# Performance work log

Measured on AMD Instinct MI355X. Metric: run time of the kernel, lower is better.

Reference implementation:

```python
import jax, jax.numpy as jnp
import numpy as np

D_MODEL = 1024
N_HEADS = 16
HEAD_DIM = D_MODEL // N_HEADS
D_FF = 4 * D_MODEL
LN_EPS = 1e-5  # torch nn.LayerNorm default


def setup_inputs() -> dict:
    key = jax.random.key(0)
    ks = jax.random.split(key, 6)
    B, T = 2, 2048
    s = lambda fan_in: 1.0 / np.sqrt(fan_in)
    return {
        "x": jax.random.normal(ks[0], (B, T, D_MODEL), dtype=jnp.float32),
        # weights stored as [in, out]
        "w_qkv": jax.random.normal(ks[1], (D_MODEL, 3 * D_MODEL), dtype=jnp.float32) * s(D_MODEL),
        "w_proj": jax.random.normal(ks[2], (D_MODEL, D_MODEL), dtype=jnp.float32) * s(D_MODEL),
        "ln1_g": jnp.ones((D_MODEL,), jnp.float32),
        "ln1_b": jnp.zeros((D_MODEL,), jnp.float32),
        "ln2_g": jnp.ones((D_MODEL,), jnp.float32),
        "ln2_b": jnp.zeros((D_MODEL,), jnp.float32),
        "w_ff1": jax.random.normal(ks[3], (D_MODEL, D_FF), dtype=jnp.float32) * s(D_MODEL),
        "b_ff1": jnp.zeros((D_FF,), jnp.float32),
        "w_ff2": jax.random.normal(ks[4], (D_FF, D_MODEL), dtype=jnp.float32) * s(D_FF),
        "b_ff2": jnp.zeros((D_MODEL,), jnp.float32),
    }


def _layernorm(x, g, b):
    mu = jnp.mean(x, axis=-1, keepdims=True)
    var = jnp.mean(jnp.square(x - mu), axis=-1, keepdims=True)
    return (x - mu) * jax.lax.rsqrt(var + LN_EPS) * g + b


def _attention(x, w_qkv, w_proj):
    B, T, C = x.shape
    qkv = x @ w_qkv  # [B,T,3C]
    q, k, v = jnp.split(qkv, 3, axis=-1)
    # [B, H, T, Dh]
    q = q.reshape(B, T, N_HEADS, HEAD_DIM).transpose(0, 2, 1, 3)
    k = k.reshape(B, T, N_HEADS, HEAD_DIM).transpose(0, 2, 1, 3)
    v = v.reshape(B, T, N_HEADS, HEAD_DIM).transpose(0, 2, 1, 3)
    att = jnp.einsum("bhqd,bhkd->bhqk", q, k) / np.sqrt(HEAD_DIM).astype(np.float32)
    causal = jnp.tril(jnp.ones((T, T), dtype=bool))
    att = jnp.where(causal, att, -jnp.inf)
    att = jax.nn.softmax(att, axis=-1)
    y = jnp.einsum("bhqk,bhkd->bhqd", att, v)
    y = y.transpose(0, 2, 1, 3).reshape(B, T, C)
    return y @ w_proj


def _ffn(x, w1, b1, w2, b2):
    h = jax.nn.gelu(x @ w1 + b1, approximate=False)  # torch nn.GELU default is exact
    return h @ w2 + b2


def reference(x, w_qkv, w_proj, ln1_g, ln1_b, ln2_g, ln2_b, w_ff1, b_ff1, w_ff2, b_ff2):
    x = x + _attention(_layernorm(x, ln1_g, ln1_b), w_qkv, w_proj)
    x = x + _ffn(_layernorm(x, ln2_g, ln2_b), w_ff1, b_ff1, w_ff2, b_ff2)
    return x
```

## Files before the change

kernel.cpp:

```cpp
#include <hip/hip_runtime.h>
#include <hip/hip_bf16.h>

typedef unsigned short u16;
typedef unsigned int u32;
typedef unsigned long long u64;
typedef __bf16 bf16x8 __attribute__((ext_vector_type(8)));
typedef float f32x4 __attribute__((ext_vector_type(4)));
typedef u16 u16x8 __attribute__((ext_vector_type(8)));

#define LN_EPS 1e-5f
#define SCALE_L2E 0.18033688011112042f

__device__ inline float bf2f(u16 u) { return __uint_as_float(((u32)u) << 16); }
__device__ inline u16 f2b(float f) {
    u32 u = __float_as_uint(f);
    u32 r = (u + 0x7fffu + ((u >> 16) & 1u)) >> 16;
    return (u16)r;
}
__device__ inline u32 cvtpk(float a, float b) {
    u32 r;
    asm("v_cvt_pk_bf16_f32 %0, %1, %2" : "=v"(r) : "v"(a), "v"(b));
    return r;
}

typedef __attribute__((address_space(3))) u32 as3_u32;
typedef const __attribute__((address_space(1))) u32 as1_u32;
__device__ inline void gl_lds16(const u16* g, u16* l) {
    __builtin_amdgcn_global_load_lds((as1_u32*)g, (as3_u32*)l, 16, 0, 0);
}

__global__ __launch_bounds__(256) void cast_transpose_k(const float* __restrict__ W,
                                                        u16* __restrict__ WT, int K, int N) {
    __shared__ float tile[64][65];
    int n0 = blockIdx.x * 64, k0 = blockIdx.y * 64;
    int t = threadIdx.x;
#pragma unroll
    for (int i = 0; i < 4; i++) {
        int idx = t + i * 256;
        int r = idx >> 4;
        int cq = idx & 15;
        float4 v = *reinterpret_cast<const float4*>(&W[(size_t)(k0 + r) * N + n0 + cq * 4]);
        tile[r][cq * 4 + 0] = v.x; tile[r][cq * 4 + 1] = v.y;
        tile[r][cq * 4 + 2] = v.z; tile[r][cq * 4 + 3] = v.w;
    }
    __syncthreads();
#pragma unroll
    for (int i = 0; i < 2; i++) {
        int c = t + i * 256;
        int n = c >> 3;
        int k8 = (c & 7) * 8;
        u16x8 o;
#pragma unroll
        for (int j = 0; j < 8; j++) o[j] = f2b(tile[k8 + j][n]);
        *reinterpret_cast<u16x8*>(&WT[(size_t)(n0 + n) * K + k0 + k8]) = o;
    }
}

__global__ __launch_bounds__(256) void layernorm_k(const float* __restrict__ X,
                                                   const float* __restrict__ g,
                                                   const float* __restrict__ b,
                                                   u16* __restrict__ out) {
    int row = blockIdx.x;
    int t = threadIdx.x;
    float4 v = *reinterpret_cast<const float4*>(&X[(size_t)row * 1024 + t * 4]);
    float s = v.x + v.y + v.z + v.w;
    float s2 = v.x * v.x + v.y * v.y + v.z * v.z + v.w * v.w;
#pragma unroll
    for (int o = 1; o < 64; o <<= 1) {
        s += __shfl_xor(s, o, 64);
        s2 += __shfl_xor(s2, o, 64);
    }
    __shared__ float ws[4], ws2[4];
    int wid = t >> 6, lane = t & 63;
    if (lane == 0) { ws[wid] = s; ws2[wid] = s2; }
    __syncthreads();
    float ts = ws[0] + ws[1] + ws[2] + ws[3];
    float ts2 = ws2[0] + ws2[1] + ws2[2] + ws2[3];
    float mu = ts * (1.0f / 1024.0f);
    float var = ts2 * (1.0f / 1024.0f) - mu * mu;
    float rs = rsqrtf(var + LN_EPS);
    float4 gg = *reinterpret_cast<const float4*>(&g[t * 4]);
    float4 bb = *reinterpret_cast<const float4*>(&b[t * 4]);
    u16 o4[4];
    o4[0] = f2b((v.x - mu) * rs * gg.x + bb.x);
    o4[1] = f2b((v.y - mu) * rs * gg.y + bb.y);
    o4[2] = f2b((v.z - mu) * rs * gg.z + bb.z);
    o4[3] = f2b((v.w - mu) * rs * gg.w + bb.w);
    *reinterpret_cast<ulonglong1*>(&out[(size_t)row * 1024 + t * 4]) =
        *reinterpret_cast<ulonglong1*>(o4);
}

__global__ __launch_bounds__(512, 2) void gemm256_k(const u16* __restrict__ A,
                                                    const u16* __restrict__ Bt,
                                                    int M, int N, int K,
                                                    const float* __restrict__ bias,
                                                    int do_gelu,
                                                    u16* __restrict__ outB) {
    __shared__ u16 As[2][256 * 64];
    __shared__ u16 Bs[2][256 * 64];
    int gx = gridDim.x;
    int nwg = gx * gridDim.y;
    int id = blockIdx.y * gx + blockIdx.x;
    int id2 = (nwg & 7) ? id : ((id & 7) * (nwg >> 3) + (id >> 3));
    int bx = id2 % gx, by = id2 / gx;
    int m0 = by * 256, n0 = bx * 256;
    int t = threadIdx.x;
    int w = t >> 6, lane = t & 63;
    int lr = lane & 15, lg = lane >> 4;
    int wm = (w >> 2) * 128, wn = (w & 3) * 64;
    f32x4 acc[8][4] = {};

    auto stage = [&](int buf, int kt) {
        int k0 = kt * 64;
#pragma unroll
        for (int i = 0; i < 4; i++) {
            int c = t + i * 512;
            int row = c >> 3, pch = c & 7;
            gl_lds16(&A[(size_t)(m0 + row) * K + k0 + ((pch ^ (row & 7)) * 8)],
                     &As[buf][c * 8]);
        }
#pragma unroll
        for (int i = 0; i < 4; i++) {
            int c = t + i * 512;
            int row = c >> 3, pch = c & 7;
            gl_lds16(&Bt[(size_t)(n0 + row) * K + k0 + ((pch ^ (row & 7)) * 8)],
                     &Bs[buf][c * 8]);
        }
    };

    int nk = K >> 6;
    stage(0, 0);
    __syncthreads();
    for (int kt = 0; kt < nk; kt++) {
        int cur = kt & 1;
        if (kt + 1 < nk) stage(cur ^ 1, kt + 1);
#pragma unroll
        for (int ks = 0; ks < 2; ks++) {
            bf16x8 af[8], bfr[4];
#pragma unroll
            for (int mi = 0; mi < 8; mi++) {
                int row = wm + mi * 16 + lr;
                af[mi] = *reinterpret_cast<const bf16x8*>(
                    &As[cur][row * 64 + (((ks * 4 + lg) ^ (row & 7)) * 8)]);
            }
#pragma unroll
            for (int ni = 0; ni < 4; ni++) {
                int row = wn + ni * 16 + lr;
                bfr[ni] = *reinterpret_cast<const bf16x8*>(
                    &Bs[cur][row * 64 + (((ks * 4 + lg) ^ (row & 7)) * 8)]);
            }
            __builtin_amdgcn_s_setprio(1);
#pragma unroll
            for (int mi = 0; mi < 8; mi++)
#pragma unroll
                for (int ni = 0; ni < 4; ni++)
                    acc[mi][ni] = __builtin_amdgcn_mfma_f32_16x16x32_bf16(
                        af[mi], bfr[ni], acc[mi][ni], 0, 0, 0);
            __builtin_amdgcn_s_setprio(0);
        }
        __syncthreads();
    }

#pragma unroll
    for (int mi = 0; mi < 8; mi++) {
#pragma unroll
        for (int ni = 0; ni < 4; ni++) {
            int col = n0 + wn + ni * 16 + lr;
#pragma unroll
            for (int i = 0; i < 4; i++) {
                int row = m0 + wm + mi * 16 + lg * 4 + i;
                float v = acc[mi][ni][i];
                if (bias) v += bias[col];
                if (do_gelu) v = 0.5f * v * (1.0f + erff(v * 0.70710678118f));
                outB[(size_t)row * N + col] = f2b(v);
            }
        }
    }
}

__global__ __launch_bounds__(256) void gemm_k(const u16* __restrict__ A,
                                              const u16* __restrict__ Bt,
                                              int M, int N, int K,
                                              const float* __restrict__ bias,
                                              const float* __restrict__ resid,
                                              int do_gelu,
                                              float* __restrict__ outF,
                                              u16* __restrict__ outB) {
    __shared__ u16 As[2][128 * 64];
    __shared__ u16 Bs[2][64 * 64];
    int gx = gridDim.x;
    int nwg = gx * gridDim.y;
    int id = blockIdx.y * gx + blockIdx.x;
    int id2 = (nwg & 7) ? id : ((id & 7) * (nwg >> 3) + (id >> 3));
    int bx = id2 % gx, by = id2 / gx;
    int m0 = by * 128, n0 = bx * 64;
    int t = threadIdx.x;
    int w = t >> 6, lane = t & 63;
    int lr = lane & 15, lg = lane >> 4;
    int wm = (w >> 1) * 64, wn = (w & 1) * 32;
    f32x4 acc[4][2] = {};

    auto stage = [&](int buf, int kt) {
        int k0 = kt * 64;
#pragma unroll
        for (int i = 0; i < 4; i++) {
            int c = t + i * 256;
            int row = c >> 3, pch = c & 7;
            gl_lds16(&A[(size_t)(m0 + row) * K + k0 + ((pch ^ (row & 7)) * 8)],
                     &As[buf][c * 8]);
        }
#pragma unroll
        for (int i = 0; i < 2; i++) {
            int c = t + i * 256;
            int row = c >> 3, pch = c & 7;
            gl_lds16(&Bt[(size_t)(n0 + row) * K + k0 + ((pch ^ (row & 7)) * 8)],
                     &Bs[buf][c * 8]);
        }
    };

    int nk = K >> 6;
    stage(0, 0);
    __syncthreads();
    for (int kt = 0; kt < nk; kt++) {
        int cur = kt & 1;
        if (kt + 1 < nk) stage(cur ^ 1, kt + 1);
#pragma unroll
        for (int ks = 0; ks < 2; ks++) {
            bf16x8 af[4], bfr[2];
#pragma unroll
            for (int mi = 0; mi < 4; mi++) {
                int row = wm + mi * 16 + lr;
                af[mi] = *reinterpret_cast<const bf16x8*>(
                    &As[cur][row * 64 + (((ks * 4 + lg) ^ (row & 7)) * 8)]);
            }
#pragma unroll
            for (int ni = 0; ni < 2; ni++) {
                int row = wn + ni * 16 + lr;
                bfr[ni] = *reinterpret_cast<const bf16x8*>(
                    &Bs[cur][row * 64 + (((ks * 4 + lg) ^ (row & 7)) * 8)]);
            }
            __builtin_amdgcn_s_setprio(1);
#pragma unroll
            for (int mi = 0; mi < 4; mi++)
#pragma unroll
                for (int ni = 0; ni < 2; ni++)
                    acc[mi][ni] = __builtin_amdgcn_mfma_f32_16x16x32_bf16(
                        af[mi], bfr[ni], acc[mi][ni], 0, 0, 0);
            __builtin_amdgcn_s_setprio(0);
        }
        __syncthreads();
    }
#pragma unroll
    for (int mi = 0; mi < 4; mi++) {
#pragma unroll
        for (int ni = 0; ni < 2; ni++) {
            int col = n0 + wn + ni * 16 + lr;
#pragma unroll
            for (int i = 0; i < 4; i++) {
                int row = m0 + wm + mi * 16 + lg * 4 + i;
                float v = acc[mi][ni][i];
                if (bias) v += bias[col];
                if (do_gelu) v = 0.5f * v * (1.0f + erff(v * 0.70710678118f));
                if (resid) v += resid[(size_t)row * N + col];
                if (outF) outF[(size_t)row * N + col] = v;
                else outB[(size_t)row * N + col] = f2b(v);
            }
        }
    }
}

__global__ __launch_bounds__(256) void attn_k(const u16* __restrict__ QKV, u16* __restrict__ Y) {
    __shared__ u16 Ks[64 * 64];
    __shared__ u16 Vt[64 * 64];
    __shared__ u16 Pt[4][16 * 64];
    int u = (blockIdx.x + blockIdx.y) & 31;
    int vv = (u & 8) ? (u ^ 7) : u;
    int qt = 31 - vv;
    int bh = blockIdx.y;
    int b = bh >> 4, h = bh & 15;
    int t = threadIdx.x;
    int w = t >> 6, lane = t & 63;
    int lr = lane & 15, lg = lane >> 4;
    int q_g = qt * 64 + w * 16 + lr;
    size_t bhbase = (size_t)b * 2048 * 3072 + h * 64;

    bf16x8 qf[2];
#pragma unroll
    for (int ks = 0; ks < 2; ks++)
        qf[ks] = *reinterpret_cast<const bf16x8*>(&QKV[bhbase + (size_t)q_g * 3072 + ks * 32 + lg * 8]);

    float l = 0.0f;
    f32x4 oacc[4] = {};

    int vkey = t & 63;
    int vd0 = (t >> 6) * 8;
    int nkv = qt + 1;

    for (int kt = 0; kt < nkv; kt++) {
        size_t tb = bhbase + (size_t)(kt * 64) * 3072;
#pragma unroll
        for (int i = 0; i < 2; i++) {
            int c = t + i * 256;
            int key = c >> 3, pch = c & 7;
            gl_lds16(&QKV[tb + (size_t)key * 3072 + 1024 + ((pch ^ (key & 7)) * 8)], &Ks[c * 8]);
        }
        u16x8 vreg[2];
#pragma unroll
        for (int i = 0; i < 2; i++)
            vreg[i] = *reinterpret_cast<const u16x8*>(&QKV[tb + (size_t)vkey * 3072 + 2048 + vd0 + i * 32]);
#pragma unroll
        for (int i = 0; i < 2; i++)
#pragma unroll
            for (int j = 0; j < 8; j++) {
                int d = vd0 + i * 32 + j;
                Vt[(d * 64 + vkey) ^ ((d & 7) << 3)] = vreg[i][j];
            }
        __syncthreads();

        int kbmax = (kt == qt) ? (w + 1) : 4;
        f32x4 s[4];
        __builtin_amdgcn_s_setprio(1);
#pragma unroll
        for (int kb = 0; kb < 4; kb++) {
            if (kb < kbmax) {
                int key = kb * 16 + lr;
                bf16x8 k0 = *reinterpret_cast<const bf16x8*>(&Ks[key * 64 + ((lg ^ (key & 7)) * 8)]);
                bf16x8 k1 = *reinterpret_cast<const bf16x8*>(&Ks[key * 64 + (((4 + lg) ^ (key & 7)) * 8)]);
                f32x4 z = {0, 0, 0, 0};
                z = __builtin_amdgcn_mfma_f32_16x16x32_bf16(k0, qf[0], z, 0, 0, 0);
                s[kb] = __builtin_amdgcn_mfma_f32_16x16x32_bf16(k1, qf[1], z, 0, 0, 0);
            }
        }
        __builtin_amdgcn_s_setprio(0);

        float p[16];
        float ps4[4];
        bool diag = (kt == qt);
#pragma unroll
        for (int kb = 0; kb < 4; kb++) {
            ps4[kb] = 0.0f;
            if (kb < kbmax) {
#pragma unroll
                for (int i2 = 0; i2 < 4; i2++) {
                    float v = s[kb][i2] * SCALE_L2E;
                    if (diag && kb == w)
                        v = (kb * 16 + lg * 4 + i2 <= w * 16 + lr) ? v : -1e30f;
                    p[kb * 4 + i2] = exp2f(v);
                }
                ps4[kb] = (p[kb * 4 + 0] + p[kb * 4 + 1]) + (p[kb * 4 + 2] + p[kb * 4 + 3]);
            }
        }
        float ps = (ps4[0] + ps4[1]) + (ps4[2] + ps4[3]);
        ps += __shfl_xor(ps, 16, 64);
        ps += __shfl_xor(ps, 32, 64);
        l += ps;
#pragma unroll
        for (int kb = 0; kb < 4; kb++) {
            u32 d0 = 0, d1 = 0;
            if (kb < kbmax) {
                d0 = cvtpk(p[kb * 4 + 0], p[kb * 4 + 1]);
                d1 = cvtpk(p[kb * 4 + 2], p[kb * 4 + 3]);
            }
            int eidx = (lr * 64 + kb * 16 + lg * 4) ^ ((lr & 7) << 3);
            *reinterpret_cast<u64*>(&Pt[w][eidx]) = (u64)d0 | ((u64)d1 << 32);
        }
        __builtin_amdgcn_s_setprio(1);
#pragma unroll
        for (int ks = 0; ks < 2; ks++) {
            bf16x8 pb = *reinterpret_cast<const bf16x8*>(&Pt[w][(lr * 64 + ks * 32 + lg * 8) ^ ((lr & 7) << 3)]);
#pragma unroll
            for (int db = 0; db < 4; db++) {
                int d = db * 16 + lr;
                bf16x8 va = *reinterpret_cast<const bf16x8*>(&Vt[(d * 64 + ks * 32 + lg * 8) ^ ((d & 7) << 3)]);
                oacc[db] = __builtin_amdgcn_mfma_f32_16x16x32_bf16(va, pb, oacc[db], 0, 0, 0);
            }
        }
        __builtin_amdgcn_s_setprio(0);
        __syncthreads();
    }

    float inv = 1.0f / l;
#pragma unroll
    for (int db = 0; db < 4; db++) {
        u32 lo = cvtpk(oacc[db][0] * inv, oacc[db][1] * inv);
        u32 hi = cvtpk(oacc[db][2] * inv, oacc[db][3] * inv);
        size_t ya = (size_t)(b * 2048 + q_g) * 1024 + h * 64 + db * 16 + lg * 4;
        *reinterpret_cast<u32*>(&Y[ya]) = lo;
        *reinterpret_cast<u32*>(&Y[ya + 2]) = hi;
    }
}

extern "C" void kernel_launch(void* const* d_in, const int* in_sizes, int n_in,
                              void* d_out, int out_size, void* d_ws, size_t ws_size,
                              hipStream_t stream) {
    const float* x      = (const float*)d_in[0];
    const float* w_qkv  = (const float*)d_in[1];
    const float* w_proj = (const float*)d_in[2];
    const float* ln1_g  = (const float*)d_in[3];
    const float* ln1_b  = (const float*)d_in[4];
    const float* ln2_g  = (const float*)d_in[5];
    const float* ln2_b  = (const float*)d_in[6];
    const float* w_ff1  = (const float*)d_in[7];
    const float* b_ff1  = (const float*)d_in[8];
    const float* w_ff2  = (const float*)d_in[9];
    const float* b_ff2  = (const float*)d_in[10];
    float* out = (float*)d_out;

    char* ws = (char*)d_ws;
    u16* qkv    = (u16*)(ws);
    u16* act16  = (u16*)(ws + 25165824);
    float* x2   = (float*)(ws + 33554432);
    u16* hbuf   = (u16*)(ws + 50331648);
    u16* wqkvT  = (u16*)(ws + 83886080);
    u16* wprojT = (u16*)(ws + 90177536);
    u16* wff1T  = (u16*)(ws + 92274688);
    u16* wff2T  = (u16*)(ws + 100663296);

    cast_transpose_k<<<dim3(48, 16), 256, 0, stream>>>(w_qkv, wqkvT, 1024, 3072);
    cast_transpose_k<<<dim3(16, 16), 256, 0, stream>>>(w_proj, wprojT, 1024, 1024);
    cast_transpose_k<<<dim3(64, 16), 256, 0, stream>>>(w_ff1, wff1T, 1024, 4096);
    cast_transpose_k<<<dim3(16, 64), 256, 0, stream>>>(w_ff2, wff2T, 4096, 1024);

    layernorm_k<<<4096, 256, 0, stream>>>(x, ln1_g, ln1_b, act16);
    gemm256_k<<<dim3(12, 16), 512, 0, stream>>>(act16, wqkvT, 4096, 3072, 1024,
                                                nullptr, 0, qkv);
    attn_k<<<dim3(32, 32), 256, 0, stream>>>(qkv, act16);
    gemm_k<<<dim3(16, 32), 256, 0, stream>>>(act16, wprojT, 4096, 1024, 1024,
                                             nullptr, x, 0, x2, nullptr);
    layernorm_k<<<4096, 256, 0, stream>>>(x2, ln2_g, ln2_b, act16);
    gemm256_k<<<dim3(16, 16), 512, 0, stream>>>(act16, wff1T, 4096, 4096, 1024,
                                                b_ff1, 1, hbuf);
    gemm_k<<<dim3(16, 32), 256, 0, stream>>>(hbuf, wff2T, 4096, 1024, 4096,
                                             b_ff2, x2, 0, out, nullptr);
}
```

Before: 304.0 us.

## Restructure 256x256 GEMM mainloop into 8-wave ping-pong with split staged loads

Rewrites the bf16 GEMM main loop as four interleaved phases. Each phase loads a quarter of the A/B fragments from LDS, issues a half-tile global-to-LDS prefetch (A for the next k-tile, B two k-tiles ahead), then runs a block of MFMAs. Explicit barriers, waitcnts and sched_barriers enforce the ordering. The aim is to overlap global loads, LDS reads and MFMA work more finely and to cut register pressure from fragments. The cost is many more barriers per k-step and fragile manual vmcnt accounting.

```diff
diff --git a/kernel.cpp b/kernel.cpp
--- a/kernel.cpp
+++ b/kernel.cpp
@@ -110,55 +110,126 @@
     int wm = (w >> 2) * 128, wn = (w & 3) * 64;
     f32x4 acc[8][4] = {};
 
-    auto stage = [&](int buf, int kt) {
+    auto stageA = [&](int buf, int kt, int h) {
         int k0 = kt * 64;
 #pragma unroll
-        for (int i = 0; i < 4; i++) {
+        for (int i = 0; i < 2; i++) {
             int c = t + i * 512;
-            int row = c >> 3, pch = c & 7;
+            int row = h * 128 + (c >> 3), pch = c & 7;
             gl_lds16(&A[(size_t)(m0 + row) * K + k0 + ((pch ^ (row & 7)) * 8)],
-                     &As[buf][c * 8]);
-        }
-#pragma unroll
-        for (int i = 0; i < 4; i++) {
+                     &As[buf][h * 8192 + c * 8]);
+        }
+    };
+    auto stageB = [&](int buf, int kt, int h) {
+        int k0 = kt * 64;
+#pragma unroll
+        for (int i = 0; i < 2; i++) {
             int c = t + i * 512;
-            int row = c >> 3, pch = c & 7;
+            int row = h * 128 + (c >> 3), pch = c & 7;
             gl_lds16(&Bt[(size_t)(n0 + row) * K + k0 + ((pch ^ (row & 7)) * 8)],
-                     &Bs[buf][c * 8]);
+                     &Bs[buf][h * 8192 + c * 8]);
         }
     };
 
     int nk = K >> 6;
-    stage(0, 0);
-    __syncthreads();
+    stageA(0, 0, 0); stageA(0, 0, 1); stageB(0, 0, 0); stageB(0, 0, 1);
+    stageB(1, 1, 0); stageB(1, 1, 1);
+    asm volatile("s_waitcnt vmcnt(4)" ::: "memory");
+    __builtin_amdgcn_s_barrier();
+    __builtin_amdgcn_sched_barrier(0);
+
     for (int kt = 0; kt < nk; kt++) {
         int cur = kt & 1;
-        if (kt + 1 < nk) stage(cur ^ 1, kt + 1);
-#pragma unroll
-        for (int ks = 0; ks < 2; ks++) {
-            bf16x8 af[8], bfr[4];
-#pragma unroll
-            for (int mi = 0; mi < 8; mi++) {
-                int row = wm + mi * 16 + lr;
-                af[mi] = *reinterpret_cast<const bf16x8*>(
-                    &As[cur][row * 64 + (((ks * 4 + lg) ^ (row & 7)) * 8)]);
-            }
-#pragma unroll
-            for (int ni = 0; ni < 4; ni++) {
-                int row = wn + ni * 16 + lr;
-                bfr[ni] = *reinterpret_cast<const bf16x8*>(
-                    &Bs[cur][row * 64 + (((ks * 4 + lg) ^ (row & 7)) * 8)]);
-            }
-            __builtin_amdgcn_s_setprio(1);
-#pragma unroll
-            for (int mi = 0; mi < 8; mi++)
-#pragma unroll
-                for (int ni = 0; ni < 4; ni++)
-                    acc[mi][ni] = __builtin_amdgcn_mfma_f32_16x16x32_bf16(
-                        af[mi], bfr[ni], acc[mi][ni], 0, 0, 0);
-            __builtin_amdgcn_s_setprio(0);
-        }
-        __syncthreads();
+        bf16x8 af[4], bfr[4][2];
+#pragma unroll
+        for (int mi = 0; mi < 4; mi++) {
+            int row = wm + mi * 16 + lr;
+            af[mi] = *reinterpret_cast<const bf16x8*>(
+                &As[cur][row * 64 + ((lg ^ (row & 7)) * 8)]);
+        }
+#pragma unroll
+        for (int ni = 0; ni < 4; ni++) {
+            int row = wn + ni * 16 + lr;
+            bfr[ni][0] = *reinterpret_cast<const bf16x8*>(
+                &Bs[cur][row * 64 + ((lg ^ (row & 7)) * 8)]);
+            bfr[ni][1] = *reinterpret_cast<const bf16x8*>(
+                &Bs[cur][row * 64 + (((4 + lg) ^ (row & 7)) * 8)]);
+        }
+        if (kt + 1 < nk) stageA(cur ^ 1, kt + 1, 0);
+        __builtin_amdgcn_s_barrier();
+        asm volatile("s_waitcnt lgkmcnt(0)" ::: "memory");
+        __builtin_amdgcn_sched_barrier(0);
+        __builtin_amdgcn_s_setprio(1);
+#pragma unroll
+        for (int mi = 0; mi < 4; mi++)
+#pragma unroll
+            for (int ni = 0; ni < 4; ni++)
+                acc[mi][ni] = __builtin_amdgcn_mfma_f32_16x16x32_bf16(
+                    af[mi], bfr[ni][0], acc[mi][ni], 0, 0, 0);
+        __builtin_amdgcn_s_setprio(0);
+        __builtin_amdgcn_s_barrier();
+        __builtin_amdgcn_sched_barrier(0);
+#pragma unroll
+        for (int mi = 0; mi < 4; mi++) {
+            int row = wm + mi * 16 + lr;
+            af[mi] = *reinterpret_cast<const bf16x8*>(
+                &As[cur][row * 64 + (((4 + lg) ^ (row & 7)) * 8)]);
+        }
+        if (kt + 1 < nk) stageA(cur ^ 1, kt + 1, 1);
+        __builtin_amdgcn_s_barrier();
+        asm volatile("s_waitcnt lgkmcnt(0)" ::: "memory");
+        __builtin_amdgcn_sched_barrier(0);
+        __builtin_amdgcn_s_setprio(1);
+#pragma unroll
+        for (int mi = 0; mi < 4; mi++)
+#pragma unroll
+            for (int ni = 0; ni < 4; ni++)
+                acc[mi][ni] = __builtin_amdgcn_mfma_f32_16x16x32_bf16(
+                    af[mi], bfr[ni][1], acc[mi][ni], 0, 0, 0);
+        __builtin_amdgcn_s_setprio(0);
+        __builtin_amdgcn_s_barrier();
+        __builtin_amdgcn_sched_barrier(0);
+#pragma unroll
+        for (int mi = 0; mi < 4; mi++) {
+            int row = wm + 64 + mi * 16 + lr;
+            af[mi] = *reinterpret_cast<const bf16x8*>(
+                &As[cur][row * 64 + ((lg ^ (row & 7)) * 8)]);
+        }
+        if (kt + 2 < nk) stageB(cur, kt + 2, 0);
+        __builtin_amdgcn_s_barrier();
+        asm volatile("s_waitcnt lgkmcnt(0)" ::: "memory");
+        __builtin_amdgcn_sched_barrier(0);
+        __builtin_amdgcn_s_setprio(1);
+#pragma unroll
+        for (int mi = 0; mi < 4; mi++)
+#pragma unroll
+            for (int ni = 0; ni < 4; ni++)
+                acc[4 + mi][ni] = __builtin_amdgcn_mfma_f32_16x16x32_bf16(
+                    af[mi], bfr[ni][0], acc[4 + mi][ni], 0, 0, 0);
+        __builtin_amdgcn_s_setprio(0);
+        __builtin_amdgcn_s_barrier();
+        __builtin_amdgcn_sched_barrier(0);
+#pragma unroll
+        for (int mi = 0; mi < 4; mi++) {
+            int row = wm + 64 + mi * 16 + lr;
+            af[mi] = *reinterpret_cast<const bf16x8*>(
+                &As[cur][row * 64 + (((4 + lg) ^ (row & 7)) * 8)]);
+        }
+        if (kt + 2 < nk) stageB(cur, kt + 2, 1);
+        __builtin_amdgcn_s_barrier();
+        asm volatile("s_waitcnt lgkmcnt(0)" ::: "memory");
+        __builtin_amdgcn_sched_barrier(0);
+        __builtin_amdgcn_s_setprio(1);
+#pragma unroll
+        for (int mi = 0; mi < 4; mi++)
+#pragma unroll
+            for (int ni = 0; ni < 4; ni++)
+                acc[4 + mi][ni] = __builtin_amdgcn_mfma_f32_16x16x32_bf16(
+                    af[mi], bfr[ni][1], acc[4 + mi][ni], 0, 0, 0);
+        __builtin_amdgcn_s_setprio(0);
+        asm volatile("s_waitcnt vmcnt(4)" ::: "memory");
+        __builtin_amdgcn_s_barrier();
+        __builtin_amdgcn_sched_barrier(0);
     }
 
 #pragma unroll
```

Result: no change. 298.7 us (median of 3 runs) (-1.7%).
